# Optimization experiments

Hardware: AMD Instinct MI355X
Metric: run time of the kernel (lower is better)

## Reference

```python
import jax, jax.numpy as jnp
import numpy as np

N_NODES = 100000


def gcn_conv(x, src, dst, W, b, n):
    # GCNConv: out = D^-1/2 (A + I) D^-1/2 (x @ W) + b, self-loops included in src/dst
    deg = jax.ops.segment_sum(jnp.ones_like(src, dtype=x.dtype), dst, num_segments=n)
    dinv = jnp.where(deg > 0, jax.lax.rsqrt(deg), 0.0)
    norm = dinv[src] * dinv[dst]                      # [E+N]
    h = x @ W                                         # [N, out] small GEMM first (PyG flow)
    msg = h[src] * norm[:, None]                      # gather + scale
    out = jax.ops.segment_sum(msg, dst, num_segments=n)
    return out + b


def setup_inputs() -> dict:
    key = jax.random.key(0)
    k1, k2, k3, k4 = jax.random.split(key, 4)
    F_IN, H, C, E = 128, 16, 4, 3200000
    x = jax.random.normal(k1, (N_NODES, F_IN), dtype=jnp.float32)
    edge_index = jax.random.randint(k2, (2, E), 0, N_NODES, dtype=jnp.int64)
    W1 = jax.random.normal(k3, (F_IN, H), dtype=jnp.float32) * (1.0 / np.sqrt(F_IN))
    b1 = jnp.zeros((H,), dtype=jnp.float32)
    W2 = jax.random.normal(k4, (H, C), dtype=jnp.float32) * (1.0 / np.sqrt(H))
    b2 = jnp.zeros((C,), dtype=jnp.float32)
    return {"x": x, "edge_index": edge_index, "W1": W1, "b1": b1, "W2": W2, "b2": b2}


def reference(x, edge_index, W1, b1, W2, b2):
    n = x.shape[0]
    loop = jnp.arange(n, dtype=edge_index.dtype)
    src = jnp.concatenate([edge_index[0], loop])
    dst = jnp.concatenate([edge_index[1], loop])
    h = gcn_conv(x, src, dst, W1, b1, n)
    h = jax.nn.relu(h)
    # dropout is identity in eval mode
    h = gcn_conv(h, src, dst, W2, b2, n)
    return jax.nn.log_softmax(h, axis=1)
```

## Files before the change

### kernel.cpp

```cpp
#include <hip/hip_runtime.h>
#include <stdint.h>

#define F_IN 128
#define HDIM 16
#define CDIM 4
#define BSH  8
#define BNODES 256
#define SMASK 131071
#define TILE 8192

__global__ void k_detect(const int* __restrict__ w, int* __restrict__ flag) {
    __shared__ int s_any;
    if (threadIdx.x == 0) s_any = 0;
    __syncthreads();
    int nz = 0;
    for (int k = threadIdx.x; k < 1024; k += blockDim.x) nz |= w[2 * k + 1];
    if (nz) atomicOr(&s_any, 1);
    __syncthreads();
    if (threadIdx.x == 0) *flag = (s_any == 0) ? 1 : 0;
}

__global__ void k_zero(int* __restrict__ bcnt) {
    bcnt[threadIdx.x] = 0;
}

__global__ __launch_bounds__(256) void k_bhist(const void* __restrict__ ei,
                                               const int* __restrict__ flag,
                                               int* __restrict__ bcnt,
                                               int E, int nbuk) {
    __shared__ int h[512];
    for (int b = threadIdx.x; b < 512; b += 256) h[b] = 0;
    __syncthreads();
    int stride = gridDim.x * 256;
    bool f64 = (*flag != 0);
    for (int e = blockIdx.x * 256 + threadIdx.x; e < E; e += stride) {
        int d = f64 ? (int)((const long long*)ei)[E + e] : ((const int*)ei)[E + e];
        atomicAdd(&h[d >> BSH], 1);
    }
    __syncthreads();
    for (int b = threadIdx.x; b < nbuk; b += 256)
        if (h[b]) atomicAdd(&bcnt[b], h[b]);
}

__global__ __launch_bounds__(512) void k_bscan(const int* __restrict__ bcnt,
                                               int* __restrict__ bbase,
                                               int* __restrict__ bcur,
                                               int nbuk, int E) {
    __shared__ int sd[512];
    int t = threadIdx.x;
    int own = (t < nbuk) ? bcnt[t] : 0;
    sd[t] = own;
    __syncthreads();
    for (int off = 1; off < 512; off <<= 1) {
        int x = (t >= off) ? sd[t - off] : 0;
        __syncthreads();
        sd[t] += x;
        __syncthreads();
    }
    if (t < nbuk) { int ex = sd[t] - own; bbase[t] = ex; bcur[t] = ex; }
    if (t == 0) bbase[nbuk] = E;
}

__global__ __launch_bounds__(512) void k_bscatter(const void* __restrict__ ei,
                                                  const int* __restrict__ flag,
                                                  int* __restrict__ bcur,
                                                  int* __restrict__ bpk,
                                                  int E, int nbuk) {
    __shared__ int hist[512], loff[512], rbase[512];
    __shared__ int lpk[TILE];
    __shared__ unsigned short lb[TILE];
    int tid = threadIdx.x;
    int tstart = blockIdx.x * TILE;
    int cnt = min(TILE, E - tstart);
    for (int b = tid; b < 512; b += 512) { hist[b] = 0; loff[b] = 0; }
    __syncthreads();
    bool f64 = (*flag != 0);
    for (int k = 0; k < TILE / 512; ++k) {
        int i = tid + k * 512;
        if (i < cnt) {
            int e = tstart + i, s, d;
            if (f64) {
                const long long* q = (const long long*)ei;
                s = (int)q[e]; d = (int)q[E + e];
            } else {
                const int* q = (const int*)ei;
                s = q[e]; d = q[E + e];
            }
            int b = d >> BSH;
            lpk[i] = s | ((d & (BNODES - 1)) << 17);
            lb[i] = (unsigned short)b;
            atomicAdd(&hist[b], 1);
        }
    }
    __syncthreads();
    if (tid < nbuk && hist[tid] > 0) rbase[tid] = atomicAdd(&bcur[tid], hist[tid]);
    __syncthreads();
    for (int k = 0; k < TILE / 512; ++k) {
        int i = tid + k * 512;
        if (i < cnt) {
            int b = lb[i];
            int p = rbase[b] + atomicAdd(&loff[b], 1);
            bpk[p] = lpk[i];
        }
    }
}

__global__ __launch_bounds__(256) void k_bdeg(const int* __restrict__ bbase,
                                              const int* __restrict__ bpk,
                                              float* __restrict__ dinv, int n) {
    __shared__ int cnt[BNODES];
    int b = blockIdx.x, tid = threadIdx.x;
    cnt[tid] = 0;
    __syncthreads();
    int start = bbase[b], end = bbase[b + 1];
    for (int i = start + tid; i < end; i += 256)
        atomicAdd(&cnt[bpk[i] >> 17], 1);
    __syncthreads();
    int g = b * BNODES + tid;
    if (g < n) dinv[g] = rsqrtf((float)(cnt[tid] + 1));
}

__global__ __launch_bounds__(256) void k_gemm1(const float* __restrict__ x,
                                               const float* __restrict__ W1,
                                               const float* __restrict__ dinv,
                                               float* __restrict__ h1s, int n) {
    __shared__ float sW[F_IN * HDIM];
    __shared__ float sX[16][F_IN + 4];
    for (int i = threadIdx.x; i < F_IN * HDIM; i += 256) sW[i] = W1[i];
    int row0 = blockIdx.x * 16;
    const float4* x4 = (const float4*)(x + (size_t)row0 * F_IN);
    for (int i = threadIdx.x; i < 512; i += 256) {
        int r = i >> 5, c4 = i & 31;
        if (row0 + r < n) *(float4*)&sX[r][c4 * 4] = x4[i];
    }
    __syncthreads();
    int c = threadIdx.x & 15, r = threadIdx.x >> 4;
    float acc = 0.f;
#pragma unroll
    for (int k = 0; k < F_IN; ++k) acc += sX[r][k] * sW[k * HDIM + c];
    int row = row0 + r;
    if (row < n) h1s[(size_t)row * HDIM + c] = acc * dinv[row];
}

__global__ __launch_bounds__(512) void k_bagg1(const int* __restrict__ bbase,
                                               const int* __restrict__ bpk,
                                               const float* __restrict__ h1s,
                                               const float* __restrict__ dinv,
                                               const float* __restrict__ b1,
                                               const float* __restrict__ W2,
                                               float* __restrict__ h2s, int n) {
    __shared__ float slab[BNODES * HDIM];
    int b = blockIdx.x, tid = threadIdx.x;
    for (int j = tid; j < BNODES * HDIM; j += 512) slab[j] = 0.f;
    __syncthreads();
    int start = bbase[b], end = bbase[b + 1];
    int f = tid & 15;
    int i = start + (tid >> 4);
    for (; i + 32 < end; i += 64) {
        int e0 = bpk[i], e1 = bpk[i + 32];
        float v0 = h1s[(size_t)(e0 & SMASK) * HDIM + f];
        float v1 = h1s[(size_t)(e1 & SMASK) * HDIM + f];
        atomicAdd(&slab[(e0 >> 17) * HDIM + f], v0);
        atomicAdd(&slab[(e1 >> 17) * HDIM + f], v1);
    }
    for (; i < end; i += 32) {
        int e0 = bpk[i];
        float v0 = h1s[(size_t)(e0 & SMASK) * HDIM + f];
        atomicAdd(&slab[(e0 >> 17) * HDIM + f], v0);
    }
    __syncthreads();
    if (tid < BNODES) {
        int g = b * BNODES + tid;
        if (g < n) {
            float di = dinv[g];
            float a0 = 0.f, a1 = 0.f, a2 = 0.f, a3 = 0.f;
#pragma unroll
            for (int j = 0; j < HDIM; ++j) {
                float t = fmaxf(di * (slab[tid * HDIM + j] +
                                      h1s[(size_t)g * HDIM + j]) + b1[j], 0.f);
                float4 w2 = ((const float4*)W2)[j];
                a0 += t * w2.x; a1 += t * w2.y; a2 += t * w2.z; a3 += t * w2.w;
            }
            ((float4*)h2s)[g] = make_float4(a0 * di, a1 * di, a2 * di, a3 * di);
        }
    }
}

__global__ __launch_bounds__(512) void k_bagg2(const int* __restrict__ bbase,
                                               const int* __restrict__ bpk,
                                               const float* __restrict__ h2s,
                                               const float* __restrict__ dinv,
                                               const float* __restrict__ b2,
                                               float* __restrict__ out, int n) {
    __shared__ float slab[BNODES * CDIM];
    int b = blockIdx.x, tid = threadIdx.x;
    for (int j = tid; j < BNODES * CDIM; j += 512) slab[j] = 0.f;
    __syncthreads();
    int start = bbase[b], end = bbase[b + 1];
    int c = tid & 3;
    int i = start + (tid >> 2);
    for (; i + 128 < end; i += 256) {
        int e0 = bpk[i], e1 = bpk[i + 128];
        float v0 = h2s[(size_t)(e0 & SMASK) * CDIM + c];
        float v1 = h2s[(size_t)(e1 & SMASK) * CDIM + c];
        atomicAdd(&slab[(e0 >> 17) * CDIM + c], v0);
        atomicAdd(&slab[(e1 >> 17) * CDIM + c], v1);
    }
    for (; i < end; i += 128) {
        int e0 = bpk[i];
        float v0 = h2s[(size_t)(e0 & SMASK) * CDIM + c];
        atomicAdd(&slab[(e0 >> 17) * CDIM + c], v0);
    }
    __syncthreads();
    if (tid < BNODES) {
        int g = b * BNODES + tid;
        if (g < n) {
            float di = dinv[g];
            float4 hs = ((const float4*)h2s)[g];
            float z0 = di * (slab[tid * 4 + 0] + hs.x) + b2[0];
            float z1 = di * (slab[tid * 4 + 1] + hs.y) + b2[1];
            float z2 = di * (slab[tid * 4 + 2] + hs.z) + b2[2];
            float z3 = di * (slab[tid * 4 + 3] + hs.w) + b2[3];
            float m = fmaxf(fmaxf(z0, z1), fmaxf(z2, z3));
            float s = expf(z0 - m) + expf(z1 - m) + expf(z2 - m) + expf(z3 - m);
            float l = m + logf(s);
            ((float4*)out)[g] = make_float4(z0 - l, z1 - l, z2 - l, z3 - l);
        }
    }
}

extern "C" void kernel_launch(void* const* d_in, const int* in_sizes, int n_in,
                              void* d_out, int out_size, void* d_ws, size_t ws_size,
                              hipStream_t stream) {
    const float* x  = (const float*)d_in[0];
    const void*  ei = d_in[1];
    const float* W1 = (const float*)d_in[2];
    const float* b1 = (const float*)d_in[3];
    const float* W2 = (const float*)d_in[4];
    const float* b2 = (const float*)d_in[5];
    float* out = (float*)d_out;

    int n = in_sizes[0] / F_IN;
    int E = in_sizes[1] / 2;
    int nbuk = (n + BNODES - 1) >> BSH;

    char* ws = (char*)d_ws;
    size_t off = 0;
    auto alloc = [&](size_t bytes) {
        char* p = ws + off;
        off = (off + bytes + 255) & ~(size_t)255;
        return p;
    };
    int*   flag  = (int*)alloc(256);
    int*   bcnt  = (int*)alloc(512 * 4);
    int*   bbase = (int*)alloc(513 * 4);
    int*   bcur  = (int*)alloc(512 * 4);
    float* dinv  = (float*)alloc((size_t)n * 4);
    float* h1s   = (float*)alloc((size_t)n * HDIM * 4);
    float* h2s   = (float*)alloc((size_t)n * CDIM * 4);
    int*   bpk   = (int*)alloc((size_t)E * 4);
    (void)ws_size;

    int ntiles = (E + TILE - 1) / TILE;

    hipLaunchKernelGGL(k_detect, dim3(1), dim3(256), 0, stream, (const int*)ei, flag);
    hipLaunchKernelGGL(k_zero, dim3(1), dim3(512), 0, stream, bcnt);
    hipLaunchKernelGGL(k_bhist, dim3(256), dim3(256), 0, stream,
                       ei, flag, bcnt, E, nbuk);
    hipLaunchKernelGGL(k_bscan, dim3(1), dim3(512), 0, stream, bcnt, bbase, bcur,
                       nbuk, E);
    hipLaunchKernelGGL(k_bscatter, dim3(ntiles), dim3(512), 0, stream,
                       ei, flag, bcur, bpk, E, nbuk);
    hipLaunchKernelGGL(k_bdeg, dim3(nbuk), dim3(256), 0, stream, bbase, bpk, dinv, n);
    hipLaunchKernelGGL(k_gemm1, dim3((n + 15) / 16), dim3(256), 0, stream,
                       x, W1, dinv, h1s, n);
    hipLaunchKernelGGL(k_bagg1, dim3(nbuk), dim3(512), 0, stream,
                       bbase, bpk, h1s, dinv, b1, W2, h2s, n);
    hipLaunchKernelGGL(k_bagg2, dim3(nbuk), dim3(512), 0, stream,
                       bbase, bpk, h2s, dinv, b2, out, n);
}
```

Baseline: 604.9 us.

## Halve node-bucket size to double block count and unroll edge gathers 8x

Shrinks destination buckets from 256 to 128 nodes, doubling the bucket count to about 782, so the aggregation and degree kernels launch twice as many blocks. Histogram, scan and scatter buffers are widened to 1024 entries to match. The degree and aggregation loops are unrolled 8-wide so several index loads and feature gathers are in flight before the shared-memory atomics. This trades more global atomics in the scatter phase and higher register use for better occupancy and memory-level parallelism in the gather-heavy kernels.

```diff
diff --git a/kernel.cpp b/kernel.cpp
--- a/kernel.cpp
+++ b/kernel.cpp
@@ -4,10 +4,11 @@
 #define F_IN 128
 #define HDIM 16
 #define CDIM 4
-#define BSH  8
-#define BNODES 256
+#define BSH  7
+#define BNODES 128
 #define SMASK 131071
 #define TILE 8192
+#define NBMAX 1024
 
 __global__ void k_detect(const int* __restrict__ w, int* __restrict__ flag) {
     __shared__ int s_any;
@@ -28,8 +29,8 @@
                                                const int* __restrict__ flag,
                                                int* __restrict__ bcnt,
                                                int E, int nbuk) {
-    __shared__ int h[512];
-    for (int b = threadIdx.x; b < 512; b += 256) h[b] = 0;
+    __shared__ int h[NBMAX];
+    for (int b = threadIdx.x; b < NBMAX; b += 256) h[b] = 0;
     __syncthreads();
     int stride = gridDim.x * 256;
     bool f64 = (*flag != 0);
@@ -42,16 +43,16 @@
         if (h[b]) atomicAdd(&bcnt[b], h[b]);
 }
 
-__global__ __launch_bounds__(512) void k_bscan(const int* __restrict__ bcnt,
-                                               int* __restrict__ bbase,
-                                               int* __restrict__ bcur,
-                                               int nbuk, int E) {
-    __shared__ int sd[512];
+__global__ __launch_bounds__(1024) void k_bscan(const int* __restrict__ bcnt,
+                                                int* __restrict__ bbase,
+                                                int* __restrict__ bcur,
+                                                int nbuk, int E) {
+    __shared__ int sd[1024];
     int t = threadIdx.x;
     int own = (t < nbuk) ? bcnt[t] : 0;
     sd[t] = own;
     __syncthreads();
-    for (int off = 1; off < 512; off <<= 1) {
+    for (int off = 1; off < 1024; off <<= 1) {
         int x = (t >= off) ? sd[t - off] : 0;
         __syncthreads();
         sd[t] += x;
@@ -66,13 +67,13 @@
                                                   int* __restrict__ bcur,
                                                   int* __restrict__ bpk,
                                                   int E, int nbuk) {
-    __shared__ int hist[512], loff[512], rbase[512];
+    __shared__ int hist[NBMAX], loff[NBMAX], rbase[NBMAX];
     __shared__ int lpk[TILE];
     __shared__ unsigned short lb[TILE];
     int tid = threadIdx.x;
     int tstart = blockIdx.x * TILE;
     int cnt = min(TILE, E - tstart);
-    for (int b = tid; b < 512; b += 512) { hist[b] = 0; loff[b] = 0; }
+    for (int b = tid; b < NBMAX; b += 512) { hist[b] = 0; loff[b] = 0; }
     __syncthreads();
     bool f64 = (*flag != 0);
     for (int k = 0; k < TILE / 512; ++k) {
@@ -93,7 +94,8 @@
         }
     }
     __syncthreads();
-    if (tid < nbuk && hist[tid] > 0) rbase[tid] = atomicAdd(&bcur[tid], hist[tid]);
+    for (int b = tid; b < nbuk; b += 512)
+        if (hist[b] > 0) rbase[b] = atomicAdd(&bcur[b], hist[b]);
     __syncthreads();
     for (int k = 0; k < TILE / 512; ++k) {
         int i = tid + k * 512;
@@ -110,14 +112,23 @@
                                               float* __restrict__ dinv, int n) {
     __shared__ int cnt[BNODES];
     int b = blockIdx.x, tid = threadIdx.x;
-    cnt[tid] = 0;
+    if (tid < BNODES) cnt[tid] = 0;
     __syncthreads();
     int start = bbase[b], end = bbase[b + 1];
-    for (int i = start + tid; i < end; i += 256)
-        atomicAdd(&cnt[bpk[i] >> 17], 1);
+    for (int i = start + tid; i < end; i += 256 * 8) {
+        int e[8];
+#pragma unroll
+        for (int u = 0; u < 8; ++u) {
+            int idx = i + u * 256;
+            e[u] = (idx < end) ? bpk[idx] : -1;
+        }
+#pragma unroll
+        for (int u = 0; u < 8; ++u)
+            if (e[u] >= 0) atomicAdd(&cnt[e[u] >> 17], 1);
+    }
     __syncthreads();
     int g = b * BNODES + tid;
-    if (g < n) dinv[g] = rsqrtf((float)(cnt[tid] + 1));
+    if (tid < BNODES && g < n) dinv[g] = rsqrtf((float)(cnt[tid] + 1));
 }
 
 __global__ __launch_bounds__(256) void k_gemm1(const float* __restrict__ x,
@@ -155,18 +166,20 @@
     __syncthreads();
     int start = bbase[b], end = bbase[b + 1];
     int f = tid & 15;
-    int i = start + (tid >> 4);
-    for (; i + 32 < end; i += 64) {
-        int e0 = bpk[i], e1 = bpk[i + 32];
-        float v0 = h1s[(size_t)(e0 & SMASK) * HDIM + f];
-        float v1 = h1s[(size_t)(e1 & SMASK) * HDIM + f];
-        atomicAdd(&slab[(e0 >> 17) * HDIM + f], v0);
-        atomicAdd(&slab[(e1 >> 17) * HDIM + f], v1);
-    }
-    for (; i < end; i += 32) {
-        int e0 = bpk[i];
-        float v0 = h1s[(size_t)(e0 & SMASK) * HDIM + f];
-        atomicAdd(&slab[(e0 >> 17) * HDIM + f], v0);
+    for (int i = start + (tid >> 4); i < end; i += 32 * 8) {
+        int e[8];
+        float v[8];
+#pragma unroll
+        for (int u = 0; u < 8; ++u) {
+            int idx = i + u * 32;
+            e[u] = (idx < end) ? bpk[idx] : -1;
+        }
+#pragma unroll
+        for (int u = 0; u < 8; ++u)
+            v[u] = (e[u] >= 0) ? h1s[(size_t)(e[u] & SMASK) * HDIM + f] : 0.f;
+#pragma unroll
+        for (int u = 0; u < 8; ++u)
+            if (e[u] >= 0) atomicAdd(&slab[(e[u] >> 17) * HDIM + f], v[u]);
     }
     __syncthreads();
     if (tid < BNODES) {
@@ -198,18 +211,20 @@
     __syncthreads();
     int start = bbase[b], end = bbase[b + 1];
     int c = tid & 3;
-    int i = start + (tid >> 2);
-    for (; i + 128 < end; i += 256) {
-        int e0 = bpk[i], e1 = bpk[i + 128];
-        float v0 = h2s[(size_t)(e0 & SMASK) * CDIM + c];
-        float v1 = h2s[(size_t)(e1 & SMASK) * CDIM + c];
-        atomicAdd(&slab[(e0 >> 17) * CDIM + c], v0);
-        atomicAdd(&slab[(e1 >> 17) * CDIM + c], v1);
-    }
-    for (; i < end; i += 128) {
-        int e0 = bpk[i];
-        float v0 = h2s[(size_t)(e0 & SMASK) * CDIM + c];
-        atomicAdd(&slab[(e0 >> 17) * CDIM + c], v0);
+    for (int i = start + (tid >> 2); i < end; i += 128 * 8) {
+        int e[8];
+        float v[8];
+#pragma unroll
+        for (int u = 0; u < 8; ++u) {
+            int idx = i + u * 128;
+            e[u] = (idx < end) ? bpk[idx] : -1;
+        }
+#pragma unroll
+        for (int u = 0; u < 8; ++u)
+            v[u] = (e[u] >= 0) ? h2s[(size_t)(e[u] & SMASK) * CDIM + c] : 0.f;
+#pragma unroll
+        for (int u = 0; u < 8; ++u)
+            if (e[u] >= 0) atomicAdd(&slab[(e[u] >> 17) * CDIM + c], v[u]);
     }
     __syncthreads();
     if (tid < BNODES) {
@@ -252,9 +267,9 @@
         return p;
     };
     int*   flag  = (int*)alloc(256);
-    int*   bcnt  = (int*)alloc(512 * 4);
-    int*   bbase = (int*)alloc(513 * 4);
-    int*   bcur  = (int*)alloc(512 * 4);
+    int*   bcnt  = (int*)alloc(NBMAX * 4);
+    int*   bbase = (int*)alloc((NBMAX + 1) * 4);
+    int*   bcur  = (int*)alloc(NBMAX * 4);
     float* dinv  = (float*)alloc((size_t)n * 4);
     float* h1s   = (float*)alloc((size_t)n * HDIM * 4);
     float* h2s   = (float*)alloc((size_t)n * CDIM * 4);
@@ -264,10 +279,10 @@
     int ntiles = (E + TILE - 1) / TILE;
 
     hipLaunchKernelGGL(k_detect, dim3(1), dim3(256), 0, stream, (const int*)ei, flag);
-    hipLaunchKernelGGL(k_zero, dim3(1), dim3(512), 0, stream, bcnt);
+    hipLaunchKernelGGL(k_zero, dim3(1), dim3(NBMAX), 0, stream, bcnt);
     hipLaunchKernelGGL(k_bhist, dim3(256), dim3(256), 0, stream,
                        ei, flag, bcnt, E, nbuk);
-    hipLaunchKernelGGL(k_bscan, dim3(1), dim3(512), 0, stream, bcnt, bbase, bcur,
+    hipLaunchKernelGGL(k_bscan, dim3(1), dim3(1024), 0, stream, bcnt, bbase, bcur,
                        nbuk, E);
     hipLaunchKernelGGL(k_bscatter, dim3(ntiles), dim3(512), 0, stream,
                        ei, flag, bcur, bpk, E, nbuk);
```

Measured after the change: 599.7 us. Within noise of the previous version (-0.9%).
